# Kernel optimization log

Measured on AMD Instinct MI355X. Metric: run time of the kernel, lower is better.

Reference implementation:

```python
import jax, jax.numpy as jnp
import numpy as np

B, Q, T, H, V = 8, 1, 2048, 512, 32000


def setup_inputs() -> dict:
    key = jax.random.key(0)
    k0, k1, k2, k3, k4 = jax.random.split(key, 5)
    s1 = 1.0 / np.sqrt(2 * H)
    return {
        "input_embeds": jax.random.normal(k0, (B, Q, H), dtype=jnp.float32),
        "target_embeds": jax.random.normal(k1, (B, T, H), dtype=jnp.float32),
        "input_mask": jnp.ones((B, T), dtype=jnp.float32),
        # MLP params: l1 Linear(2H->H, bias), l2 Linear(H->1, no bias)
        "w1": (jax.random.normal(k2, (H, 2 * H), dtype=jnp.float32) * s1),
        "b1": jnp.zeros((H,), dtype=jnp.float32),
        "w2": (jax.random.normal(k3, (H,), dtype=jnp.float32) * (1.0 / np.sqrt(H))),
        # decoder: Linear(H->V, no bias) -> weight [V, H]
        "decoder_weight": (jax.random.normal(k4, (V, H), dtype=jnp.float32) * 0.02),
    }


def reference(input_embeds, target_embeds, input_mask, w1, b1, w2, decoder_weight):
    h = w1.shape[0]
    # l1(cat(q, t)) == q @ W1q^T + t @ W1t^T + b1  (split first linear)
    w1q, w1t = w1[:, :h], w1[:, h:]
    q_proj = jnp.einsum('bqh,kh->bqk', input_embeds, w1q)        # [B,Q,H]
    t_proj = jnp.einsum('bth,kh->btk', target_embeds, w1t)       # [B,T,H]
    # pairwise query x target MLP scoring
    ht = jax.nn.relu(q_proj[:, :, None, :] + t_proj[:, None, :, :] + b1)  # [B,Q,T,H]
    repair_logits = jnp.einsum('bqtk,k->bqt', ht, w2)             # [B,Q,T]
    # _mask: mask*logits - 1000*(1-mask); mask [B,T] -> [B,1,T]
    mask = input_mask[:, None, :]
    repair_logits = mask * repair_logits - 1000.0 * (1.0 - mask)
    # decoder branch: query x vocab-row MLP scoring
    d_proj = jnp.einsum('vh,kh->vk', decoder_weight, w1t)         # [V,H]
    hd = jax.nn.relu(q_proj[:, :, None, :] + d_proj[None, None, :, :] + b1)  # [B,Q,V,H]
    decoder_logits = jnp.einsum('bqvk,k->bqv', hd, w2)            # [B,Q,V]
    out = jnp.concatenate([decoder_logits, repair_logits], axis=2)  # [B,Q,V+T]
    return jnp.squeeze(out, axis=1)  # Q == 1 -> [B, V+T]
```

## Files before the change

### kernel.cpp

```cpp
#include <hip/hip_runtime.h>
#include <hip/hip_bf16.h>

#define Hdim 512
#define Bdim 8
#define Tdim 2048
#define Vdim 32000
#define OUTW (Vdim + Tdim)
#define DEC_TILES (Vdim / 128)
#define REP_TILES ((Bdim * Tdim) / 128)
#define NTILES (DEC_TILES + REP_TILES)
#define PROWS (Vdim + Bdim * Tdim)

typedef __attribute__((ext_vector_type(8))) short short8;
typedef __attribute__((ext_vector_type(16))) float f32x16;

__device__ __forceinline__ unsigned bfr(float f) {
    union { float f; unsigned u; } x; x.f = f;
    return (x.u + 0x7FFFu + ((x.u >> 16) & 1u)) >> 16;
}
__device__ __forceinline__ unsigned packbf2(float a, float b) {
    __hip_bfloat162 h = __float22bfloat162_rn(make_float2(a, b));
    union { __hip_bfloat162 h; unsigned u; } c; c.h = h;
    return c.u;
}
__device__ __forceinline__ float lo16f(unsigned u) { return __uint_as_float(u << 16); }
__device__ __forceinline__ float hi16f(unsigned u) { return __uint_as_float(u & 0xffff0000u); }

union U8 { unsigned u[4]; short8 s; };
__device__ __forceinline__ short8 cvt8(const float4 f0, const float4 f1) {
    U8 r;
    r.u[0] = packbf2(f0.x, f0.y); r.u[1] = packbf2(f0.z, f0.w);
    r.u[2] = packbf2(f1.x, f1.y); r.u[3] = packbf2(f1.z, f1.w);
    return r.s;
}

#define WT_BLOCKS 128
#define QP_BLOCKS (Bdim * Hdim / 4)

__global__ __launch_bounds__(256) void prep_kernel(
    const float* __restrict__ w1, const float* __restrict__ x,
    const float* __restrict__ b1,
    unsigned short* __restrict__ wt, float* __restrict__ qp)
{
    const int bid = blockIdx.x;
    if (bid < WT_BLOCKS) {
        const int i = bid * 256 + threadIdx.x;
        const int n = i >> 6;
        const int kk = (i & 63) * 8;
        const float4* s = (const float4*)(w1 + (size_t)n * 1024 + 512 + kk);
        const float4 v0 = s[0], v1 = s[1];
        uint4 o;
        o.x = packbf2(v0.x, v0.y); o.y = packbf2(v0.z, v0.w);
        o.z = packbf2(v1.x, v1.y); o.w = packbf2(v1.z, v1.w);
        ((uint4*)wt)[i] = o;
    } else {
        const int widx = (bid - WT_BLOCKS) * 4 + (threadIdx.x >> 6);
        const int lane = threadIdx.x & 63;
        const int b = widx >> 9, k = widx & 511;
        const float4* xr = (const float4*)(x + b * Hdim);
        const float4* wr = (const float4*)(w1 + (size_t)k * 1024);
        float4 x0 = xr[lane * 2], x1 = xr[lane * 2 + 1];
        float4 w0 = wr[lane * 2], w1v = wr[lane * 2 + 1];
        float s = x0.x * w0.x + x0.y * w0.y + x0.z * w0.z + x0.w * w0.w
                + x1.x * w1v.x + x1.y * w1v.y + x1.z * w1v.z + x1.w * w1v.w;
#pragma unroll
        for (int off = 32; off > 0; off >>= 1) s += __shfl_down(s, off);
        if (lane == 0) qp[b * Hdim + k] = s + b1[k];
    }
}

__global__ __launch_bounds__(256, 3) void gemm_kernel(
    const float* __restrict__ Adec,
    const float* __restrict__ Atgt,
    const unsigned short* __restrict__ Wt,
    unsigned short* __restrict__ P)
{
    __shared__ struct { float A[128][64]; unsigned short W[128][64]; } u;

    const int tid  = threadIdx.x;
    const int lane = tid & 63;
    const int w    = tid >> 6;

    const int b = blockIdx.x;
    const int mt = (b >> 5) * 8 + (b & 7);
    if (mt >= NTILES) return;
    const int chunk = (b >> 3) & 3;
    const int n0 = chunk << 7;
    const bool is_dec = (mt < DEC_TILES);
    const int m0 = (is_dec ? mt : mt - DEC_TILES) << 7;
    const float* __restrict__ Af = is_dec ? Adec : Atgt;
    const int base = is_dec ? m0 : Vdim + m0;

    const int arow = w * 4 + (lane >> 4);
    const int achk = (lane & 15) ^ arow;
    const float* gA = Af + (size_t)(m0 + arow) * 512 + achk * 4;

    const int sr = lane >> 3;
    const int sc = (lane & 7) ^ sr;
    const unsigned short* gW = Wt + (size_t)(n0 + w * 32 + sr) * 512 + sc * 8;

    f32x16 acc00, acc01, acc10, acc11;
#pragma unroll
    for (int i = 0; i < 16; ++i) { acc00[i] = 0.f; acc01[i] = 0.f; acc10[i] = 0.f; acc11[i] = 0.f; }

    const int wm  = (w & 1) << 6;
    const int wn  = (w >> 1) << 6;
    const int l31 = lane & 31;
    const int kh  = lane >> 5;
    const int rx7  = l31 & 7;
    const int rx15 = l31 & 15;

    for (int h0 = 0; h0 < Hdim; h0 += 64) {
        __syncthreads();
#pragma unroll
        for (int j = 0; j < 8; ++j)
            __builtin_amdgcn_global_load_lds(
                (const __attribute__((address_space(1))) unsigned int*)(gA + j * 16 * 512),
                (__attribute__((address_space(3))) unsigned int*)(&u.A[j * 16 + w * 4][0]),
                16, 0, 0);
#pragma unroll
        for (int j = 0; j < 4; ++j)
            __builtin_amdgcn_global_load_lds(
                (const __attribute__((address_space(1))) unsigned int*)(gW + j * 8 * 512),
                (__attribute__((address_space(3))) unsigned int*)(&u.W[w * 32 + j * 8][0]),
                16, 0, 0);
        gA += 64; gW += 64;
        __syncthreads();
#pragma unroll
        for (int s = 0; s < 4; ++s) {
            const int g  = s * 2 + kh;
            const int p0 = ((2 * g) ^ rx15) << 2;
            const int p1 = ((2 * g + 1) ^ rx15) << 2;
            const float4 a0f0 = *(const float4*)&u.A[wm + l31][p0];
            const float4 a0f1 = *(const float4*)&u.A[wm + l31][p1];
            const float4 a1f0 = *(const float4*)&u.A[wm + l31 + 32][p0];
            const float4 a1f1 = *(const float4*)&u.A[wm + l31 + 32][p1];
            const short8 a0 = cvt8(a0f0, a0f1);
            const short8 a1 = cvt8(a1f0, a1f1);
            const int ow = ((g ^ rx7) << 3);
            const short8 b0 = *(const short8*)&u.W[wn + l31][ow];
            const short8 b1 = *(const short8*)&u.W[wn + l31 + 32][ow];
            acc00 = __builtin_amdgcn_mfma_f32_32x32x16_bf16(a0, b0, acc00, 0, 0, 0);
            acc01 = __builtin_amdgcn_mfma_f32_32x32x16_bf16(a0, b1, acc01, 0, 0, 0);
            acc10 = __builtin_amdgcn_mfma_f32_32x32x16_bf16(a1, b0, acc10, 0, 0, 0);
            acc11 = __builtin_amdgcn_mfma_f32_32x32x16_bf16(a1, b1, acc11, 0, 0, 0);
        }
    }

#pragma unroll
    for (int r = 0; r < 16; ++r) {
        const int ra2 = (r & 3) + ((r >> 2) << 3) + (kh << 2);
        const size_t r0 = (size_t)(base + wm + ra2) * 512 + n0;
        const size_t r1 = (size_t)(base + wm + 32 + ra2) * 512 + n0;
        P[r0 + wn + l31]      = (unsigned short)bfr(acc00[r]);
        P[r0 + wn + 32 + l31] = (unsigned short)bfr(acc01[r]);
        P[r1 + wn + l31]      = (unsigned short)bfr(acc10[r]);
        P[r1 + wn + 32 + l31] = (unsigned short)bfr(acc11[r]);
    }
}

#define EPI_DEC_BLOCKS (Vdim / 32)
#define EPI_REP_BLOCKS (Bdim * Tdim / 32)

__global__ __launch_bounds__(256) void epi_kernel(
    const unsigned short* __restrict__ P, const float* __restrict__ qp,
    const float* __restrict__ w2, const float* __restrict__ mask,
    float* __restrict__ out)
{
    const int blk = blockIdx.x;
    const int lane = threadIdx.x & 63;
    const int wv = threadIdx.x >> 6;
    const int c0 = lane * 8;

    const float4 w20 = *(const float4*)(w2 + c0);
    const float4 w21 = *(const float4*)(w2 + c0 + 4);

    if (blk < EPI_DEC_BLOCKS) {
        const int row0 = blk * 32 + wv * 8;
        float4 q0[8], q1[8];
#pragma unroll
        for (int b = 0; b < 8; ++b) {
            q0[b] = *(const float4*)(qp + b * Hdim + c0);
            q1[b] = *(const float4*)(qp + b * Hdim + c0 + 4);
        }
#pragma unroll
        for (int i = 0; i < 8; ++i) {
            const int row = row0 + i;
            const uint4 pv = *(const uint4*)(P + (size_t)row * 512 + c0);
            float p[8];
            p[0] = lo16f(pv.x); p[1] = hi16f(pv.x);
            p[2] = lo16f(pv.y); p[3] = hi16f(pv.y);
            p[4] = lo16f(pv.z); p[5] = hi16f(pv.z);
            p[6] = lo16f(pv.w); p[7] = hi16f(pv.w);
            float s[8];
#pragma unroll
            for (int b = 0; b < 8; ++b) {
                float t;
                t  = fmaxf(p[0] + q0[b].x, 0.f) * w20.x;
                t += fmaxf(p[1] + q0[b].y, 0.f) * w20.y;
                t += fmaxf(p[2] + q0[b].z, 0.f) * w20.z;
                t += fmaxf(p[3] + q0[b].w, 0.f) * w20.w;
                t += fmaxf(p[4] + q1[b].x, 0.f) * w21.x;
                t += fmaxf(p[5] + q1[b].y, 0.f) * w21.y;
                t += fmaxf(p[6] + q1[b].z, 0.f) * w21.z;
                t += fmaxf(p[7] + q1[b].w, 0.f) * w21.w;
                s[b] = t;
            }
#pragma unroll
            for (int off = 1; off <= 4; off <<= 1)
#pragma unroll
                for (int b = 0; b < 8; ++b) s[b] += __shfl_xor(s[b], off);
            float v = s[lane & 7];
#pragma unroll
            for (int off = 8; off <= 32; off <<= 1) v += __shfl_xor(v, off);
            if (lane < 8) out[(size_t)lane * OUTW + row] = v;
        }
    } else {
        const int rr0 = (blk - EPI_DEC_BLOCKS) * 32 + wv * 8;
        const int b = rr0 >> 11;
        const float4 q0 = *(const float4*)(qp + b * Hdim + c0);
        const float4 q1 = *(const float4*)(qp + b * Hdim + c0 + 4);
#pragma unroll
        for (int i = 0; i < 8; ++i) {
            const int rr = rr0 + i;
            const uint4 pv = *(const uint4*)(P + (size_t)(Vdim + rr) * 512 + c0);
            float p[8];
            p[0] = lo16f(pv.x); p[1] = hi16f(pv.x);
            p[2] = lo16f(pv.y); p[3] = hi16f(pv.y);
            p[4] = lo16f(pv.z); p[5] = hi16f(pv.z);
            p[6] = lo16f(pv.w); p[7] = hi16f(pv.w);
            float s;
            s  = fmaxf(p[0] + q0.x, 0.f) * w20.x;
            s += fmaxf(p[1] + q0.y, 0.f) * w20.y;
            s += fmaxf(p[2] + q0.z, 0.f) * w20.z;
            s += fmaxf(p[3] + q0.w, 0.f) * w20.w;
            s += fmaxf(p[4] + q1.x, 0.f) * w21.x;
            s += fmaxf(p[5] + q1.y, 0.f) * w21.y;
            s += fmaxf(p[6] + q1.z, 0.f) * w21.z;
            s += fmaxf(p[7] + q1.w, 0.f) * w21.w;
#pragma unroll
            for (int off = 32; off > 0; off >>= 1) s += __shfl_xor(s, off);
            if (lane == 0) {
                const int t = rr & 2047;
                const float mv = mask[b * Tdim + t];
                out[(size_t)b * OUTW + Vdim + t] = mv * s - 1000.f * (1.f - mv);
            }
        }
    }
}

extern "C" void kernel_launch(void* const* d_in, const int* in_sizes, int n_in,
                              void* d_out, int out_size, void* d_ws, size_t ws_size,
                              hipStream_t stream) {
    const float* input_embeds  = (const float*)d_in[0];
    const float* target_embeds = (const float*)d_in[1];
    const float* input_mask    = (const float*)d_in[2];
    const float* w1            = (const float*)d_in[3];
    const float* b1            = (const float*)d_in[4];
    const float* w2            = (const float*)d_in[5];
    const float* decoder_w     = (const float*)d_in[6];
    float* out = (float*)d_out;

    float* qp = (float*)d_ws;
    unsigned short* Pbuf = (unsigned short*)((char*)d_ws + 16384);
    unsigned short* wt   = Pbuf + (size_t)PROWS * Hdim;

    prep_kernel<<<WT_BLOCKS + QP_BLOCKS, 256, 0, stream>>>(w1, input_embeds, b1, wt, qp);
    gemm_kernel<<<48 * 32, 256, 0, stream>>>(decoder_w, target_embeds, wt, Pbuf);
    epi_kernel<<<EPI_DEC_BLOCKS + EPI_REP_BLOCKS, 256, 0, stream>>>(Pbuf, qp, w2, input_mask, out);
}
```

Measured before the change: 213.6 us.

## Fuse ReLU-MLP epilogue into GEMM and accumulate logits with atomics

Removes the bf16 intermediate P buffer and the separate epilogue kernel. The GEMM now swaps its MFMA operands so each lane holds one output row across many hidden columns, then applies the q-add, ReLU and w2 weighting in registers. It reduces per 128-column chunk and atomically adds partial logits into an output that the prep kernel pre-initialises (zeros, plus the mask bias for the repair part). This cuts a large write and reread of the projection matrix, at the cost of atomic contention from four column chunks per row and a heavier GEMM epilogue with more register pressure.

New measurement: 290.3 us. 1.36x slower.

```diff
diff --git a/kernel.cpp b/kernel.cpp
--- a/kernel.cpp
+++ b/kernel.cpp
@@ -9,22 +9,15 @@
 #define DEC_TILES (Vdim / 128)
 #define REP_TILES ((Bdim * Tdim) / 128)
 #define NTILES (DEC_TILES + REP_TILES)
-#define PROWS (Vdim + Bdim * Tdim)
 
 typedef __attribute__((ext_vector_type(8))) short short8;
 typedef __attribute__((ext_vector_type(16))) float f32x16;
 
-__device__ __forceinline__ unsigned bfr(float f) {
-    union { float f; unsigned u; } x; x.f = f;
-    return (x.u + 0x7FFFu + ((x.u >> 16) & 1u)) >> 16;
-}
 __device__ __forceinline__ unsigned packbf2(float a, float b) {
     __hip_bfloat162 h = __float22bfloat162_rn(make_float2(a, b));
     union { __hip_bfloat162 h; unsigned u; } c; c.h = h;
     return c.u;
 }
-__device__ __forceinline__ float lo16f(unsigned u) { return __uint_as_float(u << 16); }
-__device__ __forceinline__ float hi16f(unsigned u) { return __uint_as_float(u & 0xffff0000u); }
 
 union U8 { unsigned u[4]; short8 s; };
 __device__ __forceinline__ short8 cvt8(const float4 f0, const float4 f1) {
@@ -36,11 +29,13 @@
 
 #define WT_BLOCKS 128
 #define QP_BLOCKS (Bdim * Hdim / 4)
+#define INIT_BLOCKS (Bdim * OUTW / 4 / 256)
 
 __global__ __launch_bounds__(256) void prep_kernel(
     const float* __restrict__ w1, const float* __restrict__ x,
-    const float* __restrict__ b1,
-    unsigned short* __restrict__ wt, float* __restrict__ qp)
+    const float* __restrict__ b1, const float* __restrict__ mask,
+    unsigned short* __restrict__ wt, float* __restrict__ qp,
+    float* __restrict__ out)
 {
     const int bid = blockIdx.x;
     if (bid < WT_BLOCKS) {
@@ -53,7 +48,7 @@
         o.x = packbf2(v0.x, v0.y); o.y = packbf2(v0.z, v0.w);
         o.z = packbf2(v1.x, v1.y); o.w = packbf2(v1.z, v1.w);
         ((uint4*)wt)[i] = o;
-    } else {
+    } else if (bid < WT_BLOCKS + QP_BLOCKS) {
         const int widx = (bid - WT_BLOCKS) * 4 + (threadIdx.x >> 6);
         const int lane = threadIdx.x & 63;
         const int b = widx >> 9, k = widx & 511;
@@ -66,6 +61,20 @@
 #pragma unroll
         for (int off = 32; off > 0; off >>= 1) s += __shfl_down(s, off);
         if (lane == 0) qp[b * Hdim + k] = s + b1[k];
+    } else {
+        const int idx4 = (bid - WT_BLOCKS - QP_BLOCKS) * 256 + threadIdx.x;
+        const int b = idx4 / (OUTW / 4);
+        const int c4 = (idx4 - b * (OUTW / 4)) * 4;
+        float4 v;
+        if (c4 < Vdim) {
+            v = make_float4(0.f, 0.f, 0.f, 0.f);
+        } else {
+            const int t = c4 - Vdim;
+            const float4 mv = *(const float4*)(mask + b * Tdim + t);
+            v = make_float4(-1000.f * (1.f - mv.x), -1000.f * (1.f - mv.y),
+                            -1000.f * (1.f - mv.z), -1000.f * (1.f - mv.w));
+        }
+        ((float4*)out)[idx4] = v;
     }
 }
 
@@ -73,9 +82,15 @@
     const float* __restrict__ Adec,
     const float* __restrict__ Atgt,
     const unsigned short* __restrict__ Wt,
-    unsigned short* __restrict__ P)
+    const float* __restrict__ qp,
+    const float* __restrict__ w2,
+    const float* __restrict__ mask,
+    float* __restrict__ out)
 {
-    __shared__ struct { float A[128][64]; unsigned short W[128][64]; } u;
+    __shared__ union {
+        struct { float A[128][64]; unsigned short W[128][64]; } g;
+        struct { float q[128][8]; float w2c[128]; } e;
+    } u;
 
     const int tid  = threadIdx.x;
     const int lane = tid & 63;
@@ -89,7 +104,6 @@
     const bool is_dec = (mt < DEC_TILES);
     const int m0 = (is_dec ? mt : mt - DEC_TILES) << 7;
     const float* __restrict__ Af = is_dec ? Adec : Atgt;
-    const int base = is_dec ? m0 : Vdim + m0;
 
     const int arow = w * 4 + (lane >> 4);
     const int achk = (lane & 15) ^ arow;
@@ -116,13 +130,13 @@
         for (int j = 0; j < 8; ++j)
             __builtin_amdgcn_global_load_lds(
                 (const __attribute__((address_space(1))) unsigned int*)(gA + j * 16 * 512),
-                (__attribute__((address_space(3))) unsigned int*)(&u.A[j * 16 + w * 4][0]),
+                (__attribute__((address_space(3))) unsigned int*)(&u.g.A[j * 16 + w * 4][0]),
                 16, 0, 0);
 #pragma unroll
         for (int j = 0; j < 4; ++j)
             __builtin_amdgcn_global_load_lds(
                 (const __attribute__((address_space(1))) unsigned int*)(gW + j * 8 * 512),
-                (__attribute__((address_space(3))) unsigned int*)(&u.W[w * 32 + j * 8][0]),
+                (__attribute__((address_space(3))) unsigned int*)(&u.g.W[w * 32 + j * 8][0]),
                 16, 0, 0);
         gA += 64; gW += 64;
         __syncthreads();
@@ -131,120 +145,101 @@
             const int g  = s * 2 + kh;
             const int p0 = ((2 * g) ^ rx15) << 2;
             const int p1 = ((2 * g + 1) ^ rx15) << 2;
-            const float4 a0f0 = *(const float4*)&u.A[wm + l31][p0];
-            const float4 a0f1 = *(const float4*)&u.A[wm + l31][p1];
-            const float4 a1f0 = *(const float4*)&u.A[wm + l31 + 32][p0];
-            const float4 a1f1 = *(const float4*)&u.A[wm + l31 + 32][p1];
+            const float4 a0f0 = *(const float4*)&u.g.A[wm + l31][p0];
+            const float4 a0f1 = *(const float4*)&u.g.A[wm + l31][p1];
+            const float4 a1f0 = *(const float4*)&u.g.A[wm + l31 + 32][p0];
+            const float4 a1f1 = *(const float4*)&u.g.A[wm + l31 + 32][p1];
             const short8 a0 = cvt8(a0f0, a0f1);
             const short8 a1 = cvt8(a1f0, a1f1);
             const int ow = ((g ^ rx7) << 3);
-            const short8 b0 = *(const short8*)&u.W[wn + l31][ow];
-            const short8 b1 = *(const short8*)&u.W[wn + l31 + 32][ow];
-            acc00 = __builtin_amdgcn_mfma_f32_32x32x16_bf16(a0, b0, acc00, 0, 0, 0);
-            acc01 = __builtin_amdgcn_mfma_f32_32x32x16_bf16(a0, b1, acc01, 0, 0, 0);
-            acc10 = __builtin_amdgcn_mfma_f32_32x32x16_bf16(a1, b0, acc10, 0, 0, 0);
-            acc11 = __builtin_amdgcn_mfma_f32_32x32x16_bf16(a1, b1, acc11, 0, 0, 0);
+            const short8 b0 = *(const short8*)&u.g.W[wn + l31][ow];
+            const short8 b1 = *(const short8*)&u.g.W[wn + l31 + 32][ow];
+            acc00 = __builtin_amdgcn_mfma_f32_32x32x16_bf16(b0, a0, acc00, 0, 0, 0);
+            acc01 = __builtin_amdgcn_mfma_f32_32x32x16_bf16(b0, a1, acc01, 0, 0, 0);
+            acc10 = __builtin_amdgcn_mfma_f32_32x32x16_bf16(b1, a0, acc10, 0, 0, 0);
+            acc11 = __builtin_amdgcn_mfma_f32_32x32x16_bf16(b1, a1, acc11, 0, 0, 0);
         }
     }
 
-#pragma unroll
-    for (int r = 0; r < 16; ++r) {
-        const int ra2 = (r & 3) + ((r >> 2) << 3) + (kh << 2);
-        const size_t r0 = (size_t)(base + wm + ra2) * 512 + n0;
-        const size_t r1 = (size_t)(base + wm + 32 + ra2) * 512 + n0;
-        P[r0 + wn + l31]      = (unsigned short)bfr(acc00[r]);
-        P[r0 + wn + 32 + l31] = (unsigned short)bfr(acc01[r]);
-        P[r1 + wn + l31]      = (unsigned short)bfr(acc10[r]);
-        P[r1 + wn + 32 + l31] = (unsigned short)bfr(acc11[r]);
-    }
-}
-
-#define EPI_DEC_BLOCKS (Vdim / 32)
-#define EPI_REP_BLOCKS (Bdim * Tdim / 32)
-
-__global__ __launch_bounds__(256) void epi_kernel(
-    const unsigned short* __restrict__ P, const float* __restrict__ qp,
-    const float* __restrict__ w2, const float* __restrict__ mask,
-    float* __restrict__ out)
-{
-    const int blk = blockIdx.x;
-    const int lane = threadIdx.x & 63;
-    const int wv = threadIdx.x >> 6;
-    const int c0 = lane * 8;
-
-    const float4 w20 = *(const float4*)(w2 + c0);
-    const float4 w21 = *(const float4*)(w2 + c0 + 4);
-
-    if (blk < EPI_DEC_BLOCKS) {
-        const int row0 = blk * 32 + wv * 8;
-        float4 q0[8], q1[8];
-#pragma unroll
-        for (int b = 0; b < 8; ++b) {
-            q0[b] = *(const float4*)(qp + b * Hdim + c0);
-            q1[b] = *(const float4*)(qp + b * Hdim + c0 + 4);
-        }
-#pragma unroll
-        for (int i = 0; i < 8; ++i) {
-            const int row = row0 + i;
-            const uint4 pv = *(const uint4*)(P + (size_t)row * 512 + c0);
-            float p[8];
-            p[0] = lo16f(pv.x); p[1] = hi16f(pv.x);
-            p[2] = lo16f(pv.y); p[3] = hi16f(pv.y);
-            p[4] = lo16f(pv.z); p[5] = hi16f(pv.z);
-            p[6] = lo16f(pv.w); p[7] = hi16f(pv.w);
-            float s[8];
-#pragma unroll
-            for (int b = 0; b < 8; ++b) {
-                float t;
-                t  = fmaxf(p[0] + q0[b].x, 0.f) * w20.x;
-                t += fmaxf(p[1] + q0[b].y, 0.f) * w20.y;
-                t += fmaxf(p[2] + q0[b].z, 0.f) * w20.z;
-                t += fmaxf(p[3] + q0[b].w, 0.f) * w20.w;
-                t += fmaxf(p[4] + q1[b].x, 0.f) * w21.x;
-                t += fmaxf(p[5] + q1[b].y, 0.f) * w21.y;
-                t += fmaxf(p[6] + q1[b].z, 0.f) * w21.z;
-                t += fmaxf(p[7] + q1[b].w, 0.f) * w21.w;
-                s[b] = t;
-            }
-#pragma unroll
-            for (int off = 1; off <= 4; off <<= 1)
-#pragma unroll
-                for (int b = 0; b < 8; ++b) s[b] += __shfl_xor(s[b], off);
-            float v = s[lane & 7];
-#pragma unroll
-            for (int off = 8; off <= 32; off <<= 1) v += __shfl_xor(v, off);
-            if (lane < 8) out[(size_t)lane * OUTW + row] = v;
+    __syncthreads();
+    for (int idx = tid; idx < 1024; idx += 256)
+        ((float*)u.e.q)[idx] = qp[(idx & 7) * Hdim + n0 + (idx >> 3)];
+    if (tid < 128) u.e.w2c[tid] = w2[n0 + tid];
+    __syncthreads();
+
+    if (is_dec) {
+        float ps0[8], ps1[8];
+#pragma unroll
+        for (int b2 = 0; b2 < 8; ++b2) { ps0[b2] = 0.f; ps1[b2] = 0.f; }
+#pragma unroll
+        for (int r = 0; r < 16; ++r) {
+            const int ra2 = (r & 3) + ((r >> 2) << 3) + (kh << 2);
+            {
+                const int nl = wn + ra2;
+                float q8[8];
+                *(float4*)&q8[0] = *(const float4*)&u.e.q[nl][0];
+                *(float4*)&q8[4] = *(const float4*)&u.e.q[nl][4];
+                const float w2n = u.e.w2c[nl];
+#pragma unroll
+                for (int b2 = 0; b2 < 8; ++b2) {
+                    ps0[b2] += fmaxf(acc00[r] + q8[b2], 0.f) * w2n;
+                    ps1[b2] += fmaxf(acc01[r] + q8[b2], 0.f) * w2n;
+                }
+            }
+            {
+                const int nl = wn + 32 + ra2;
+                float q8[8];
+                *(float4*)&q8[0] = *(const float4*)&u.e.q[nl][0];
+                *(float4*)&q8[4] = *(const float4*)&u.e.q[nl][4];
+                const float w2n = u.e.w2c[nl];
+#pragma unroll
+                for (int b2 = 0; b2 < 8; ++b2) {
+                    ps0[b2] += fmaxf(acc10[r] + q8[b2], 0.f) * w2n;
+                    ps1[b2] += fmaxf(acc11[r] + q8[b2], 0.f) * w2n;
+                }
+            }
+        }
+#pragma unroll
+        for (int b2 = 0; b2 < 8; ++b2) {
+            const float t0 = ps0[b2] + __shfl_xor(ps0[b2], 32);
+            const float t1 = ps1[b2] + __shfl_xor(ps1[b2], 32);
+            if (kh == 0) {
+                float* o = out + (size_t)b2 * OUTW + m0 + wm;
+                unsafeAtomicAdd(o + l31, t0);
+                unsafeAtomicAdd(o + 32 + l31, t1);
+            }
         }
     } else {
-        const int rr0 = (blk - EPI_DEC_BLOCKS) * 32 + wv * 8;
-        const int b = rr0 >> 11;
-        const float4 q0 = *(const float4*)(qp + b * Hdim + c0);
-        const float4 q1 = *(const float4*)(qp + b * Hdim + c0 + 4);
-#pragma unroll
-        for (int i = 0; i < 8; ++i) {
-            const int rr = rr0 + i;
-            const uint4 pv = *(const uint4*)(P + (size_t)(Vdim + rr) * 512 + c0);
-            float p[8];
-            p[0] = lo16f(pv.x); p[1] = hi16f(pv.x);
-            p[2] = lo16f(pv.y); p[3] = hi16f(pv.y);
-            p[4] = lo16f(pv.z); p[5] = hi16f(pv.z);
-            p[6] = lo16f(pv.w); p[7] = hi16f(pv.w);
-            float s;
-            s  = fmaxf(p[0] + q0.x, 0.f) * w20.x;
-            s += fmaxf(p[1] + q0.y, 0.f) * w20.y;
-            s += fmaxf(p[2] + q0.z, 0.f) * w20.z;
-            s += fmaxf(p[3] + q0.w, 0.f) * w20.w;
-            s += fmaxf(p[4] + q1.x, 0.f) * w21.x;
-            s += fmaxf(p[5] + q1.y, 0.f) * w21.y;
-            s += fmaxf(p[6] + q1.z, 0.f) * w21.z;
-            s += fmaxf(p[7] + q1.w, 0.f) * w21.w;
-#pragma unroll
-            for (int off = 32; off > 0; off >>= 1) s += __shfl_xor(s, off);
-            if (lane == 0) {
-                const int t = rr & 2047;
-                const float mv = mask[b * Tdim + t];
-                out[(size_t)b * OUTW + Vdim + t] = mv * s - 1000.f * (1.f - mv);
-            }
+        const int bfix = m0 >> 11;
+        float ps0 = 0.f, ps1 = 0.f;
+#pragma unroll
+        for (int r = 0; r < 16; ++r) {
+            const int ra2 = (r & 3) + ((r >> 2) << 3) + (kh << 2);
+            {
+                const int nl = wn + ra2;
+                const float qv = u.e.q[nl][bfix];
+                const float w2n = u.e.w2c[nl];
+                ps0 += fmaxf(acc00[r] + qv, 0.f) * w2n;
+                ps1 += fmaxf(acc01[r] + qv, 0.f) * w2n;
+            }
+            {
+                const int nl = wn + 32 + ra2;
+                const float qv = u.e.q[nl][bfix];
+                const float w2n = u.e.w2c[nl];
+                ps0 += fmaxf(acc10[r] + qv, 0.f) * w2n;
+                ps1 += fmaxf(acc11[r] + qv, 0.f) * w2n;
+            }
+        }
+        const float t0 = ps0 + __shfl_xor(ps0, 32);
+        const float t1 = ps1 + __shfl_xor(ps1, 32);
+        if (kh == 0) {
+            const int t0i = (m0 & 2047) + wm + l31;
+            const int t1i = t0i + 32;
+            const float mv0 = mask[bfix * Tdim + t0i];
+            const float mv1 = mask[bfix * Tdim + t1i];
+            float* o = out + (size_t)bfix * OUTW + Vdim;
+            unsafeAtomicAdd(o + t0i, mv0 * t0);
+            unsafeAtomicAdd(o + t1i, mv1 * t1);
         }
     }
 }
@@ -262,10 +257,10 @@
     float* out = (float*)d_out;
 
     float* qp = (float*)d_ws;
-    unsigned short* Pbuf = (unsigned short*)((char*)d_ws + 16384);
-    unsigned short* wt   = Pbuf + (size_t)PROWS * Hdim;
-
-    prep_kernel<<<WT_BLOCKS + QP_BLOCKS, 256, 0, stream>>>(w1, input_embeds, b1, wt, qp);
-    gemm_kernel<<<48 * 32, 256, 0, stream>>>(decoder_w, target_embeds, wt, Pbuf);
-    epi_kernel<<<EPI_DEC_BLOCKS + EPI_REP_BLOCKS, 256, 0, stream>>>(Pbuf, qp, w2, input_mask, out);
-}
+    unsigned short* wt = (unsigned short*)((char*)d_ws + 16384);
+
+    prep_kernel<<<WT_BLOCKS + QP_BLOCKS + INIT_BLOCKS, 256, 0, stream>>>(
+        w1, input_embeds, b1, input_mask, wt, qp, out);
+    gemm_kernel<<<48 * 32, 256, 0, stream>>>(
+        decoder_w, target_embeds, wt, qp, w2, input_mask, out);
+}
```
